# Kernel tuning notes

Measured on AMD Instinct MI355X. Metric: run time of the kernel, lower is better.

## Reference

```python
import jax, jax.numpy as jnp
import numpy as np

N = 4096          # nodes
D_IN = 1024       # in_features
H = 16            # heads
DH = D_IN // H    # d_head
ALPHA = 0.2       # LeakyReLU negative slope
MASK_VAL = -65500.0


def setup_inputs() -> dict:
    key = jax.random.key(0)
    ks = jax.random.split(key, 7)
    x = jax.random.normal(ks[0], (N, D_IN), dtype=jnp.float32)
    adj = jax.random.randint(ks[1], (N, N), 0, 2).astype(jnp.float32)
    s = 1.0 / np.sqrt(D_IN)
    W_seq = jax.random.normal(ks[2], (D_IN, D_IN), dtype=jnp.float32) * s
    a1 = jax.random.normal(ks[3], (DH,), dtype=jnp.float32) / np.sqrt(DH)
    a2 = jax.random.normal(ks[4], (DH,), dtype=jnp.float32) / np.sqrt(DH)
    W_out = jax.random.normal(ks[5], (D_IN, D_IN), dtype=jnp.float32) * s
    b_out = jax.random.normal(ks[6], (D_IN,), dtype=jnp.float32) * 0.01
    return {"x": x, "adj": adj, "W_seq": W_seq, "a1": a1, "a2": a2,
            "W_out": W_out, "b_out": b_out}


def reference(x, adj, W_seq, a1, a2, W_out, b_out):
    # seq: [N, H, DH]
    seq = (x @ W_seq).reshape(N, H, DH)
    # per-head scalar scores: [H, N]
    score1 = jnp.einsum('nhd,d->hn', seq, a1)
    score2 = jnp.einsum('nhd,d->hn', seq, a2)
    # additive attention scores: [H, N, N]
    scores = score1[:, :, None] + score2[:, None, :]
    scores = jax.nn.leaky_relu(scores, negative_slope=ALPHA)
    scores = scores + (1.0 - adj)[None, :, :] * MASK_VAL
    attn = jax.nn.softmax(scores, axis=-1)          # [H, N, N]
    # dropout p=0 -> identity
    hidden = jnp.einsum('hij,jhd->ihd', attn, seq).reshape(N, D_IN)
    hidden = hidden @ W_out + b_out
    # residual=False, concat=True -> ELU
    return jax.nn.elu(hidden)
```

## Files before the change

kernel.cpp:

```cpp
#include <hip/hip_runtime.h>
#include <hip/hip_bf16.h>
#include <math.h>

#define NN 4096
#define DIN 1024
#define NH 16
#define DH 64

typedef unsigned short u16;
typedef unsigned long long u64;
typedef u16 u16x4 __attribute__((ext_vector_type(4)));
typedef u16 u16x8 __attribute__((ext_vector_type(8)));
typedef unsigned ux2 __attribute__((ext_vector_type(2)));
typedef unsigned ux4 __attribute__((ext_vector_type(4)));
typedef float fx4 __attribute__((ext_vector_type(4)));
typedef __bf16 bf16x8 __attribute__((ext_vector_type(8)));
typedef _Float16 h16x8 __attribute__((ext_vector_type(8)));

__device__ __forceinline__ u16 f2b(float f) {
  unsigned u = __float_as_uint(f);
  u += 0x7fff + ((u >> 16) & 1);
  return (u16)(u >> 16);
}
__device__ __forceinline__ float b2f(u16 h) {
  return __uint_as_float(((unsigned)h) << 16);
}
__device__ __forceinline__ u16 f2h_bits(float f) {
  _Float16 h = (_Float16)f;
  return __builtin_bit_cast(unsigned short, h);
}
__device__ __forceinline__ unsigned pack2h(float f) {
  unsigned hb = (unsigned)f2h_bits(f);
  return hb | (hb << 16);
}
__device__ __forceinline__ unsigned pk_mul(unsigned a, unsigned b) {
  unsigned d;
  asm("v_pk_mul_f16 %0, %1, %2" : "=v"(d) : "v"(a), "v"(b));
  return d;
}
__device__ __forceinline__ unsigned pk_max(unsigned a, unsigned b) {
  unsigned d;
  asm("v_pk_max_f16 %0, %1, %2" : "=v"(d) : "v"(a), "v"(b));
  return d;
}
__device__ __forceinline__ void gload16(const void* g, void* l) {
  __builtin_amdgcn_global_load_lds(
      (const __attribute__((address_space(1))) unsigned*)g,
      (__attribute__((address_space(3))) unsigned*)l, 16, 0, 0);
}
__device__ __forceinline__ void wait_vm6() {
  asm volatile("s_waitcnt vmcnt(6)" ::: "memory");
}

__global__ __launch_bounds__(256) void cast_kernel(const float* __restrict__ in,
                                                   u16* __restrict__ out, int n4) {
  int i = blockIdx.x * 256 + threadIdx.x;
  if (i < n4) {
    fx4 v = reinterpret_cast<const fx4*>(in)[i];
    u16x4 o;
    o[0] = f2b(v[0]); o[1] = f2b(v[1]); o[2] = f2b(v[2]); o[3] = f2b(v[3]);
    reinterpret_cast<u16x4*>(out)[i] = o;
  }
}

__global__ __launch_bounds__(256) void tcast_kernel(const float* __restrict__ in,
                                                    u16* __restrict__ out, int R, int C) {
  __shared__ u16 tile[32][33];
  int bc = blockIdx.x * 32, br = blockIdx.y * 32;
  int tx = threadIdx.x & 31, ty = threadIdx.x >> 5;
  #pragma unroll
  for (int r = ty; r < 32; r += 8)
    tile[r][tx] = f2b(in[(size_t)(br + r) * C + bc + tx]);
  __syncthreads();
  #pragma unroll
  for (int r = ty; r < 32; r += 8)
    out[(size_t)(bc + r) * R + br + tx] = tile[tx][r];
}

__global__ __launch_bounds__(256, 2) void gemm_seq(const u16* __restrict__ A,
                                                   const u16* __restrict__ BT,
                                                   const float* __restrict__ a1,
                                                   const float* __restrict__ a2,
                                                   u16* __restrict__ seqTh,
                                                   float* __restrict__ s1T,
                                                   float* __restrict__ s2H,
                                                   int K) {
  __shared__ __align__(16) u16 As[2][128 * 64];
  __shared__ __align__(16) u16 Bs[2][64 * 64];
  const int tid = threadIdx.x;
  const int i0 = blockIdx.x * 128, n0 = blockIdx.y * 64, h = blockIdx.y;
  const int w = tid >> 6, l = tid & 63;
  const int wr = w >> 1, wc = w & 1;
  const int lr = l & 15, lslot = l >> 4;
  const int wu = __builtin_amdgcn_readfirstlane(w);
  const int srow_lo = l >> 3, sg = (l & 7) ^ (srow_lo & 7);
  const u16* gA[4];
  #pragma unroll
  for (int jj = 0; jj < 4; jj++)
    gA[jj] = A + (size_t)(i0 + wu * 32 + jj * 8 + srow_lo) * K + sg * 8;
  const u16* gB[2];
  #pragma unroll
  for (int jb = 0; jb < 2; jb++)
    gB[jb] = BT + (size_t)(n0 + wu * 16 + jb * 8 + srow_lo) * K + sg * 8;

  fx4 acc[4][2] = {};

  #pragma unroll
  for (int jj = 0; jj < 4; jj++)
    gload16(gA[jj], (char*)As[0] + wu * 4096 + jj * 1024);
  #pragma unroll
  for (int jb = 0; jb < 2; jb++)
    gload16(gB[jb], (char*)Bs[0] + wu * 2048 + jb * 1024);
  __syncthreads();

  for (int kt = 0; kt < 16; kt++) {
    const int buf = kt & 1;
    __builtin_amdgcn_s_barrier();
    {
      const int kn = ((kt + 1) & 15) * 64;
      __builtin_amdgcn_sched_barrier(0);
      #pragma unroll
      for (int jj = 0; jj < 4; jj++)
        gload16(gA[jj] + kn, (char*)As[buf ^ 1] + wu * 4096 + jj * 1024);
      #pragma unroll
      for (int jb = 0; jb < 2; jb++)
        gload16(gB[jb] + kn, (char*)Bs[buf ^ 1] + wu * 2048 + jb * 1024);
      __builtin_amdgcn_sched_barrier(0);
      wait_vm6();
      __builtin_amdgcn_sched_barrier(0);
    }
    __builtin_amdgcn_s_barrier();
    #pragma unroll
    for (int ks = 0; ks < 2; ks++) {
      bf16x8 af[4], bfr[2];
      #pragma unroll
      for (int mi = 0; mi < 4; mi++) {
        const int r = wr * 64 + mi * 16 + lr;
        const int sl = (ks * 4 + lslot) ^ (r & 7);
        af[mi] = *reinterpret_cast<const bf16x8*>((const char*)As[buf] + r * 128 + sl * 16);
      }
      #pragma unroll
      for (int ni = 0; ni < 2; ni++) {
        const int r = wc * 32 + ni * 16 + lr;
        const int sl = (ks * 4 + lslot) ^ (r & 7);
        bfr[ni] = *reinterpret_cast<const bf16x8*>((const char*)Bs[buf] + r * 128 + sl * 16);
      }
      #pragma unroll
      for (int mi = 0; mi < 4; mi++)
        #pragma unroll
        for (int ni = 0; ni < 2; ni++)
          acc[mi][ni] = __builtin_amdgcn_mfma_f32_16x16x32_bf16(af[mi], bfr[ni], acc[mi][ni], 0, 0, 0);
    }
  }
  __syncthreads();

  float a1v[2], a2v[2];
  #pragma unroll
  for (int ni = 0; ni < 2; ni++) {
    int dl = wc * 32 + ni * 16 + lr;
    a1v[ni] = a1[dl];
    a2v[ni] = a2[dl];
  }
  #pragma unroll
  for (int mi = 0; mi < 4; mi++)
    #pragma unroll
    for (int r = 0; r < 4; r++) {
      float s1 = acc[mi][0][r] * a1v[0] + acc[mi][1][r] * a1v[1];
      float s2 = acc[mi][0][r] * a2v[0] + acc[mi][1][r] * a2v[1];
      #pragma unroll
      for (int off = 1; off < 16; off <<= 1) {
        s1 += __shfl_xor(s1, off);
        s2 += __shfl_xor(s2, off);
      }
      if (lr == 0) {
        int row = i0 + wr * 64 + mi * 16 + lslot * 4 + r;
        atomicAdd(&s1T[row * NH + h], s1);
        atomicAdd(&s2H[(size_t)h * NN + row], s2);
      }
    }

  u16* tp = (u16*)As;
  #pragma unroll
  for (int mi = 0; mi < 4; mi++)
    #pragma unroll
    for (int ni = 0; ni < 2; ni++)
      #pragma unroll
      for (int rp = 0; rp < 2; rp++) {
        unsigned pw = (unsigned)f2h_bits(acc[mi][ni][2 * rp]) |
                      ((unsigned)f2h_bits(acc[mi][ni][2 * rp + 1]) << 16);
        int d = wc * 32 + ni * 16 + lr;
        int i = wr * 64 + mi * 16 + lslot * 4 + 2 * rp;
        *reinterpret_cast<unsigned*>(&tp[d * 132 + i]) = pw;
      }
  __syncthreads();
  const int dd = tid >> 2, ic = (tid & 3) * 32;
  u16* go = seqTh + (size_t)(h * DH + dd) * NN + i0 + ic;
  #pragma unroll
  for (int q = 0; q < 8; q++) {
    u16x4 v = *reinterpret_cast<const u16x4*>(&tp[dd * 132 + ic + q * 4]);
    *reinterpret_cast<u16x4*>(go + q * 4) = v;
  }
}

__global__ __launch_bounds__(256, 2) void gemm_bt(const u16* __restrict__ A,
                                                  const u16* __restrict__ BT,
                                                  float* __restrict__ Cf,
                                                  const float* __restrict__ bias,
                                                  int M, int N, int K) {
  __shared__ __align__(16) u16 As[2][128 * 64];
  __shared__ __align__(16) u16 Bs[2][64 * 64];
  const int tid = threadIdx.x;
  const int i0 = blockIdx.x * 128, n0 = blockIdx.y * 64;
  const int w = tid >> 6, l = tid & 63;
  const int wr = w >> 1, wc = w & 1;
  const int lr = l & 15, lslot = l >> 4;
  const int wu = __builtin_amdgcn_readfirstlane(w);
  const int srow_lo = l >> 3, sg = (l & 7) ^ (srow_lo & 7);
  const u16* gA[4];
  #pragma unroll
  for (int jj = 0; jj < 4; jj++)
    gA[jj] = A + (size_t)(i0 + wu * 32 + jj * 8 + srow_lo) * K + sg * 8;
  const u16* gB[2];
  #pragma unroll
  for (int jb = 0; jb < 2; jb++)
    gB[jb] = BT + (size_t)(n0 + wu * 16 + jb * 8 + srow_lo) * K + sg * 8;

  fx4 acc[4][2] = {};

  #pragma unroll
  for (int jj = 0; jj < 4; jj++)
    gload16(gA[jj], (char*)As[0] + wu * 4096 + jj * 1024);
  #pragma unroll
  for (int jb = 0; jb < 2; jb++)
    gload16(gB[jb], (char*)Bs[0] + wu * 2048 + jb * 1024);
  __syncthreads();

  for (int kt = 0; kt < 16; kt++) {
    const int buf = kt & 1;
    __builtin_amdgcn_s_barrier();
    {
      const int kn = ((kt + 1) & 15) * 64;
      __builtin_amdgcn_sched_barrier(0);
      #pragma unroll
      for (int jj = 0; jj < 4; jj++)
        gload16(gA[jj] + kn, (char*)As[buf ^ 1] + wu * 4096 + jj * 1024);
      #pragma unroll
      for (int jb = 0; jb < 2; jb++)
        gload16(gB[jb] + kn, (char*)Bs[buf ^ 1] + wu * 2048 + jb * 1024);
      __builtin_amdgcn_sched_barrier(0);
      wait_vm6();
      __builtin_amdgcn_sched_barrier(0);
    }
    __builtin_amdgcn_s_barrier();
    #pragma unroll
    for (int ks = 0; ks < 2; ks++) {
      bf16x8 af[4], bfr[2];
      #pragma unroll
      for (int mi = 0; mi < 4; mi++) {
        const int r = wr * 64 + mi * 16 + lr;
        const int sl = (ks * 4 + lslot) ^ (r & 7);
        af[mi] = *reinterpret_cast<const bf16x8*>((const char*)As[buf] + r * 128 + sl * 16);
      }
      #pragma unroll
      for (int ni = 0; ni < 2; ni++) {
        const int r = wc * 32 + ni * 16 + lr;
        const int sl = (ks * 4 + lslot) ^ (r & 7);
        bfr[ni] = *reinterpret_cast<const bf16x8*>((const char*)Bs[buf] + r * 128 + sl * 16);
      }
      #pragma unroll
      for (int mi = 0; mi < 4; mi++)
        #pragma unroll
        for (int ni = 0; ni < 2; ni++)
          acc[mi][ni] = __builtin_amdgcn_mfma_f32_16x16x32_bf16(af[mi], bfr[ni], acc[mi][ni], 0, 0, 0);
    }
  }

  const int orow = wr * 64 + lslot * 4;
  const int ocol = wc * 32 + lr;
  #pragma unroll
  for (int mi = 0; mi < 4; mi++)
    #pragma unroll
    for (int r = 0; r < 4; r++)
      #pragma unroll
      for (int ni = 0; ni < 2; ni++) {
        int col = n0 + ocol + ni * 16;
        float v = acc[mi][ni][r] + bias[col];
        Cf[(size_t)(i0 + orow + mi * 16 + r) * N + col] = v > 0.f ? v : expm1f(v);
      }
}

__global__ __launch_bounds__(256) void prep_kernel(const float* __restrict__ s2H,
                                                   float* __restrict__ Dmax,
                                                   unsigned* __restrict__ epH2,
                                                   unsigned* __restrict__ enH2) {
  __shared__ float red[4];
  __shared__ float sDm;
  const int h = blockIdx.x, t = threadIdx.x;
  const fx4* d = reinterpret_cast<const fx4*>(s2H + (size_t)h * NN);
  fx4 v[4];
  float mx = -3e38f;
  #pragma unroll
  for (int q = 0; q < 4; q++) {
    v[q] = d[t * 4 + q];
    #pragma unroll
    for (int z = 0; z < 4; z++) mx = fmaxf(mx, v[q][z]);
  }
  #pragma unroll
  for (int off = 1; off < 64; off <<= 1) mx = fmaxf(mx, __shfl_xor(mx, off));
  if ((t & 63) == 0) red[t >> 6] = mx;
  __syncthreads();
  if (t == 0) {
    float m = fmaxf(fmaxf(red[0], red[1]), fmaxf(red[2], red[3]));
    sDm = m;
    Dmax[h] = m;
  }
  __syncthreads();
  const float Dm = sDm;
  #pragma unroll
  for (int q = 0; q < 8; q++) {
    float d0 = v[q >> 1][(q & 1) * 2];
    float d1 = v[q >> 1][(q & 1) * 2 + 1];
    unsigned ep = (unsigned)f2h_bits(__expf(d0 - Dm)) |
                  ((unsigned)f2h_bits(__expf(d1 - Dm)) << 16);
    unsigned en = (unsigned)f2h_bits(__expf(0.2f * (d0 - Dm))) |
                  ((unsigned)f2h_bits(__expf(0.2f * (d1 - Dm))) << 16);
    epH2[h * 2048 + t * 8 + q] = ep;
    enH2[h * 2048 + t * 8 + q] = en;
  }
}

__global__ __launch_bounds__(256) void maskb_kernel(const float* __restrict__ adj,
                                                    unsigned char* __restrict__ mb) {
  size_t g = (size_t)blockIdx.x * 256 + threadIdx.x;
  const fx4* ap = reinterpret_cast<const fx4*>(adj) + g * 4;
  ux4 o;
  #pragma unroll
  for (int q = 0; q < 4; q++) {
    fx4 a = ap[q];
    unsigned b0 = a[0] > 0.5f ? 0xFFu : 0u;
    unsigned b1 = a[1] > 0.5f ? 0xFFu : 0u;
    unsigned b2 = a[2] > 0.5f ? 0xFFu : 0u;
    unsigned b3 = a[3] > 0.5f ? 0xFFu : 0u;
    o[q] = b0 | (b1 << 8) | (b2 << 16) | (b3 << 24);
  }
  reinterpret_cast<ux4*>(mb)[g] = o;
}

__device__ __forceinline__ h16x8 build_p(unsigned Ai2, unsigned Bi2,
                                         ux4 ep, ux4 en, ux2 mk) {
  unsigned w0 = __builtin_amdgcn_perm(0u, mk[0], 0x01010000u);
  unsigned w1 = __builtin_amdgcn_perm(0u, mk[0], 0x03030202u);
  unsigned w2 = __builtin_amdgcn_perm(0u, mk[1], 0x01010000u);
  unsigned w3 = __builtin_amdgcn_perm(0u, mk[1], 0x03030202u);
  ux4 afw;
  afw[0] = pk_max(pk_mul(Ai2, ep[0]), pk_mul(Bi2, en[0])) & w0;
  afw[1] = pk_max(pk_mul(Ai2, ep[1]), pk_mul(Bi2, en[1])) & w1;
  afw[2] = pk_max(pk_mul(Ai2, ep[2]), pk_mul(Bi2, en[2])) & w2;
  afw[3] = pk_max(pk_mul(Ai2, ep[3]), pk_mul(Bi2, en[3])) & w3;
  return __builtin_bit_cast(h16x8, afw);
}

__global__ __launch_bounds__(512, 4) void pv_kernel(const unsigned char* __restrict__ maskB,
                                                    const u16* __restrict__ seqTh,
                                                    const float* __restrict__ s1T,
                                                    const float* __restrict__ Dmax,
                                                    const unsigned* __restrict__ epH2,
                                                    const unsigned* __restrict__ enH2,
                                                    u16* __restrict__ hiddenb) {
  __shared__ __align__(16) u16 Vs[2][64 * 128];
  __shared__ __align__(16) unsigned epL[2048];
  __shared__ __align__(16) unsigned enL[2048];
  const int h = blockIdx.x >> 5, it = blockIdx.x & 31, i0 = it * 128;
  const int t = threadIdx.x, w = t >> 6, l = t & 63;
  const int lr = l & 15, hi = l >> 4, lk = hi * 8;
  const float Dm = Dmax[h];
  const int arow = i0 + w * 16 + lr;
  const float c = s1T[arow * NH + h];
  float mi = c + Dm;
  mi = mi > 0.f ? mi : 0.2f * mi;
  const unsigned Ai2 = pack2h(__expf(c + Dm - mi));
  const unsigned Bi2 = pack2h(__expf(0.2f * (c + Dm) - mi));
  {
    const ux4* gep = reinterpret_cast<const ux4*>(epH2 + h * 2048);
    const ux4* gen = reinterpret_cast<const ux4*>(enH2 + h * 2048);
    ux4 e0 = gep[t];
    ux4 n0 = gen[t];
    *reinterpret_cast<ux4*>(&epL[t * 4]) = e0;
    *reinterpret_cast<ux4*>(&enL[t * 4]) = n0;
  }
  const int wu = __builtin_amdgcn_readfirstlane(w);
  const u16* gsrc[2];
  #pragma unroll
  for (int i = 0; i < 2; i++) {
    int row = wu * 8 + i * 4 + (l >> 4);
    int g = (l & 15) ^ (row & 7);
    gsrc[i] = seqTh + (size_t)(h * DH + row) * NN + g * 8;
  }
  const unsigned char* gm0 = maskB + (size_t)arow * NN + lk;
  fx4 acc[4] = {};
  fx4 acc1 = {};
  h16x8 ones;
  #pragma unroll
  for (int e = 0; e < 8; e++) ones[e] = (_Float16)1.0f;

  #pragma unroll
  for (int i = 0; i < 2; i++)
    gload16(gsrc[i], (char*)Vs[0] + wu * 2048 + i * 1024);
  ux2 mkc[2][2], mkn[2][2];
  #pragma unroll
  for (int jj = 0; jj < 2; jj++)
    #pragma unroll
    for (int ks = 0; ks < 2; ks++)
      mkc[jj][ks] = *reinterpret_cast<const ux2*>(gm0 + jj * 64 + ks * 32);
  __syncthreads();

  for (int JT = 0; JT < 32; JT++) {
    const int buf = JT & 1;
    __builtin_amdgcn_s_barrier();
    {
      const int jn = ((JT + 1) & 31) * 128;
      __builtin_amdgcn_sched_barrier(0);
      #pragma unroll
      for (int i = 0; i < 2; i++)
        gload16(gsrc[i] + jn, (char*)Vs[buf ^ 1] + wu * 2048 + i * 1024);
      #pragma unroll
      for (int jj = 0; jj < 2; jj++)
        #pragma unroll
        for (int ks = 0; ks < 2; ks++)
          mkn[jj][ks] = *reinterpret_cast<const ux2*>(gm0 + jn + jj * 64 + ks * 32);
      __builtin_amdgcn_sched_barrier(0);
      wait_vm6();
      __builtin_amdgcn_sched_barrier(0);
    }
    __builtin_amdgcn_s_barrier();
    #pragma unroll
    for (int jj = 0; jj < 2; jj++) {
      #pragma unroll
      for (int ks = 0; ks < 2; ks++) {
        const int jp = JT * 64 + jj * 32 + ks * 16 + hi * 4;
        ux4 ep = *reinterpret_cast<const ux4*>(&epL[jp]);
        ux4 en = *reinterpret_cast<const ux4*>(&enL[jp]);
        h16x8 bfr[4];
        #pragma unroll
        for (int ni = 0; ni < 4; ni++) {
          const int row = ni * 16 + lr;
          const int colb = (jj * 128 + ks * 64 + hi * 16) ^ ((lr & 7) << 4);
          bfr[ni] = *reinterpret_cast<const h16x8*>((const char*)Vs[buf] + row * 256 + colb);
        }
        h16x8 A = build_p(Ai2, Bi2, ep, en, mkc[jj][ks]);
        #pragma unroll
        for (int ni = 0; ni < 4; ni++)
          acc[ni] = __builtin_amdgcn_mfma_f32_16x16x32_f16(A, bfr[ni], acc[ni], 0, 0, 0);
        acc1 = __builtin_amdgcn_mfma_f32_16x16x32_f16(A, ones, acc1, 0, 0, 0);
      }
    }
    #pragma unroll
    for (int jj = 0; jj < 2; jj++)
      #pragma unroll
      for (int ks = 0; ks < 2; ks++)
        mkc[jj][ks] = mkn[jj][ks];
  }

  #pragma unroll
  for (int r = 0; r < 4; r++) {
    int row = i0 + w * 16 + hi * 4 + r;
    float inv = 1.0f / acc1[r];
    #pragma unroll
    for (int ni = 0; ni < 4; ni++)
      hiddenb[(size_t)row * DIN + h * DH + ni * 16 + lr] = f2b(acc[ni][r] * inv);
  }
}

extern "C" void kernel_launch(void* const* d_in, const int* in_sizes, int n_in,
                              void* d_out, int out_size, void* d_ws, size_t ws_size,
                              hipStream_t stream) {
  const float* x = (const float*)d_in[0];
  const float* adj = (const float*)d_in[1];
  const float* W_seq = (const float*)d_in[2];
  const float* a1 = (const float*)d_in[3];
  const float* a2 = (const float*)d_in[4];
  const float* W_out = (const float*)d_in[5];
  const float* b_out = (const float*)d_in[6];

  char* ws = (char*)d_ws;
  u16* wsT   = (u16*)(ws);
  u16* woT   = (u16*)(ws + (2u << 20));
  u16* seqTh = (u16*)(ws + (12u << 20));
  u16* hid   = (u16*)(ws + (20u << 20));
  float* s1T = (float*)(ws + (28u << 20));
  float* s2H = s1T + NN * NH;
  unsigned* epH2 = (unsigned*)(s2H + NN * NH);
  unsigned* enH2 = epH2 + NH * 2048;
  float* DmaxB = (float*)(enH2 + NH * 2048);
  u16* xb = (u16*)(ws + (29u << 20));
  unsigned char* maskB = (unsigned char*)(ws + (29u << 20));

  cast_kernel<<<4096, 256, 0, stream>>>(x, xb, NN * DIN / 4);
  tcast_kernel<<<dim3(32, 32), 256, 0, stream>>>(W_seq, wsT, DIN, DIN);
  tcast_kernel<<<dim3(32, 32), 256, 0, stream>>>(W_out, woT, DIN, DIN);
  hipMemsetAsync(s1T, 0, 2u * NN * NH * sizeof(float), stream);
  gemm_seq<<<dim3(32, 16), 256, 0, stream>>>(xb, wsT, a1, a2, seqTh, s1T, s2H, DIN);
  prep_kernel<<<16, 256, 0, stream>>>(s2H, DmaxB, epH2, enH2);
  maskb_kernel<<<4096, 256, 0, stream>>>(adj, maskB);
  pv_kernel<<<512, 512, 0, stream>>>(maskB, seqTh, s1T, DmaxB, epH2, enH2, hid);
  gemm_bt<<<dim3(32, 16), 256, 0, stream>>>(hid, woT, (float*)d_out, b_out, NN, DIN, DIN);
}
```

Baseline: 148.6 us.

## Process two row tiles per wave in PV kernel to reuse V fragments

Each wave in the attention-times-V kernel now handles 32 query rows (two 16-row M tiles) instead of 16. This halves the grid to 256 blocks and reuses each V fragment read from LDS across two MFMA chains. The main loop is unrolled by two with explicit ping-pong buffers, which removes the mask register copy, and the waitcnt is raised to match the larger number of outstanding loads. The cost is higher register pressure (launch bounds drop to 2 blocks per CU) and only 256 blocks, which may underfill the MI355X's 256 CUs.

```diff
diff --git a/kernel.cpp b/kernel.cpp
--- a/kernel.cpp
+++ b/kernel.cpp
@@ -50,6 +50,9 @@
 }
 __device__ __forceinline__ void wait_vm6() {
   asm volatile("s_waitcnt vmcnt(6)" ::: "memory");
+}
+__device__ __forceinline__ void wait_vm10() {
+  asm volatile("s_waitcnt vmcnt(10)" ::: "memory");
 }
 
 __global__ __launch_bounds__(256) void cast_kernel(const float* __restrict__ in,
@@ -360,7 +363,7 @@
   return __builtin_bit_cast(h16x8, afw);
 }
 
-__global__ __launch_bounds__(512, 4) void pv_kernel(const unsigned char* __restrict__ maskB,
+__global__ __launch_bounds__(512, 2) void pv_kernel(const unsigned char* __restrict__ maskB,
                                                     const u16* __restrict__ seqTh,
                                                     const float* __restrict__ s1T,
                                                     const float* __restrict__ Dmax,
@@ -370,16 +373,22 @@
   __shared__ __align__(16) u16 Vs[2][64 * 128];
   __shared__ __align__(16) unsigned epL[2048];
   __shared__ __align__(16) unsigned enL[2048];
-  const int h = blockIdx.x >> 5, it = blockIdx.x & 31, i0 = it * 128;
+  const int h = blockIdx.x >> 4, it = blockIdx.x & 15, i0 = it * 256;
   const int t = threadIdx.x, w = t >> 6, l = t & 63;
   const int lr = l & 15, hi = l >> 4, lk = hi * 8;
   const float Dm = Dmax[h];
-  const int arow = i0 + w * 16 + lr;
-  const float c = s1T[arow * NH + h];
-  float mi = c + Dm;
-  mi = mi > 0.f ? mi : 0.2f * mi;
-  const unsigned Ai2 = pack2h(__expf(c + Dm - mi));
-  const unsigned Bi2 = pack2h(__expf(0.2f * (c + Dm) - mi));
+  unsigned Ai2[2], Bi2[2];
+  int arow[2];
+  #pragma unroll
+  for (int m = 0; m < 2; m++) {
+    int row = i0 + w * 32 + m * 16 + lr;
+    arow[m] = row;
+    float c = s1T[row * NH + h];
+    float mi = c + Dm;
+    mi = mi > 0.f ? mi : 0.2f * mi;
+    Ai2[m] = pack2h(__expf(c + Dm - mi));
+    Bi2[m] = pack2h(__expf(0.2f * (c + Dm) - mi));
+  }
   {
     const ux4* gep = reinterpret_cast<const ux4*>(epH2 + h * 2048);
     const ux4* gen = reinterpret_cast<const ux4*>(enH2 + h * 2048);
@@ -396,43 +405,34 @@
     int g = (l & 15) ^ (row & 7);
     gsrc[i] = seqTh + (size_t)(h * DH + row) * NN + g * 8;
   }
-  const unsigned char* gm0 = maskB + (size_t)arow * NN + lk;
-  fx4 acc[4] = {};
-  fx4 acc1 = {};
+  const unsigned char* gm[2];
+  gm[0] = maskB + (size_t)arow[0] * NN + lk;
+  gm[1] = maskB + (size_t)arow[1] * NN + lk;
+  fx4 acc[2][4] = {};
+  fx4 acc1[2] = {};
   h16x8 ones;
   #pragma unroll
   for (int e = 0; e < 8; e++) ones[e] = (_Float16)1.0f;
 
-  #pragma unroll
-  for (int i = 0; i < 2; i++)
-    gload16(gsrc[i], (char*)Vs[0] + wu * 2048 + i * 1024);
-  ux2 mkc[2][2], mkn[2][2];
-  #pragma unroll
-  for (int jj = 0; jj < 2; jj++)
-    #pragma unroll
-    for (int ks = 0; ks < 2; ks++)
-      mkc[jj][ks] = *reinterpret_cast<const ux2*>(gm0 + jj * 64 + ks * 32);
-  __syncthreads();
-
-  for (int JT = 0; JT < 32; JT++) {
-    const int buf = JT & 1;
-    __builtin_amdgcn_s_barrier();
-    {
-      const int jn = ((JT + 1) & 31) * 128;
-      __builtin_amdgcn_sched_barrier(0);
-      #pragma unroll
-      for (int i = 0; i < 2; i++)
-        gload16(gsrc[i] + jn, (char*)Vs[buf ^ 1] + wu * 2048 + i * 1024);
+  ux2 mkA[2][2][2], mkB[2][2][2];
+
+  auto issue = [&](int JTn, u16* vbuf, ux2 (&mk)[2][2][2]) {
+    const int jn = JTn * 128;
+    __builtin_amdgcn_sched_barrier(0);
+    #pragma unroll
+    for (int i = 0; i < 2; i++)
+      gload16(gsrc[i] + jn, (char*)vbuf + wu * 2048 + i * 1024);
+    #pragma unroll
+    for (int m = 0; m < 2; m++)
       #pragma unroll
       for (int jj = 0; jj < 2; jj++)
         #pragma unroll
         for (int ks = 0; ks < 2; ks++)
-          mkn[jj][ks] = *reinterpret_cast<const ux2*>(gm0 + jn + jj * 64 + ks * 32);
-      __builtin_amdgcn_sched_barrier(0);
-      wait_vm6();
-      __builtin_amdgcn_sched_barrier(0);
-    }
-    __builtin_amdgcn_s_barrier();
+          mk[m][jj][ks] = *reinterpret_cast<const ux2*>(gm[m] + jn + jj * 64 + ks * 32);
+    __builtin_amdgcn_sched_barrier(0);
+  };
+
+  auto compute = [&](int JT, const u16* vbuf, const ux2 (&mk)[2][2][2]) {
     #pragma unroll
     for (int jj = 0; jj < 2; jj++) {
       #pragma unroll
@@ -445,30 +445,49 @@
         for (int ni = 0; ni < 4; ni++) {
           const int row = ni * 16 + lr;
           const int colb = (jj * 128 + ks * 64 + hi * 16) ^ ((lr & 7) << 4);
-          bfr[ni] = *reinterpret_cast<const h16x8*>((const char*)Vs[buf] + row * 256 + colb);
+          bfr[ni] = *reinterpret_cast<const h16x8*>((const char*)vbuf + row * 256 + colb);
         }
-        h16x8 A = build_p(Ai2, Bi2, ep, en, mkc[jj][ks]);
         #pragma unroll
-        for (int ni = 0; ni < 4; ni++)
-          acc[ni] = __builtin_amdgcn_mfma_f32_16x16x32_f16(A, bfr[ni], acc[ni], 0, 0, 0);
-        acc1 = __builtin_amdgcn_mfma_f32_16x16x32_f16(A, ones, acc1, 0, 0, 0);
-      }
-    }
-    #pragma unroll
-    for (int jj = 0; jj < 2; jj++)
-      #pragma unroll
-      for (int ks = 0; ks < 2; ks++)
-        mkc[jj][ks] = mkn[jj][ks];
-  }
-
-  #pragma unroll
-  for (int r = 0; r < 4; r++) {
-    int row = i0 + w * 16 + hi * 4 + r;
-    float inv = 1.0f / acc1[r];
-    #pragma unroll
-    for (int ni = 0; ni < 4; ni++)
-      hiddenb[(size_t)row * DIN + h * DH + ni * 16 + lr] = f2b(acc[ni][r] * inv);
-  }
+        for (int m = 0; m < 2; m++) {
+          h16x8 A = build_p(Ai2[m], Bi2[m], ep, en, mk[m][jj][ks]);
+          #pragma unroll
+          for (int ni = 0; ni < 4; ni++)
+            acc[m][ni] = __builtin_amdgcn_mfma_f32_16x16x32_f16(A, bfr[ni], acc[m][ni], 0, 0, 0);
+          acc1[m] = __builtin_amdgcn_mfma_f32_16x16x32_f16(A, ones, acc1[m], 0, 0, 0);
+        }
+      }
+    }
+  };
+
+  issue(0, Vs[0], mkA);
+  __syncthreads();
+
+  for (int JT2 = 0; JT2 < 16; JT2++) {
+    const int JTa = JT2 * 2, JTb = JTa + 1;
+    __builtin_amdgcn_s_barrier();
+    issue(JTb, Vs[1], mkB);
+    wait_vm10();
+    __builtin_amdgcn_sched_barrier(0);
+    __builtin_amdgcn_s_barrier();
+    compute(JTa, Vs[0], mkA);
+    __builtin_amdgcn_s_barrier();
+    issue((JTb + 1) & 31, Vs[0], mkA);
+    wait_vm10();
+    __builtin_amdgcn_sched_barrier(0);
+    __builtin_amdgcn_s_barrier();
+    compute(JTb, Vs[1], mkB);
+  }
+
+  #pragma unroll
+  for (int m = 0; m < 2; m++)
+    #pragma unroll
+    for (int r = 0; r < 4; r++) {
+      int row = i0 + w * 32 + m * 16 + hi * 4 + r;
+      float inv = 1.0f / acc1[m][r];
+      #pragma unroll
+      for (int ni = 0; ni < 4; ni++)
+        hiddenb[(size_t)row * DIN + h * DH + ni * 16 + lr] = f2b(acc[m][ni][r] * inv);
+    }
 }
 
 extern "C" void kernel_launch(void* const* d_in, const int* in_sizes, int n_in,
@@ -502,6 +521,6 @@
   gemm_seq<<<dim3(32, 16), 256, 0, stream>>>(xb, wsT, a1, a2, seqTh, s1T, s2H, DIN);
   prep_kernel<<<16, 256, 0, stream>>>(s2H, DmaxB, epH2, enH2);
   maskb_kernel<<<4096, 256, 0, stream>>>(adj, maskB);
-  pv_kernel<<<512, 512, 0, stream>>>(maskB, seqTh, s1T, DmaxB, epH2, enH2, hid);
+  pv_kernel<<<256, 512, 0, stream>>>(maskB, seqTh, s1T, DmaxB, epH2, enH2, hid);
   gemm_bt<<<dim3(32, 16), 256, 0, stream>>>(hid, woT, (float*)d_out, b_out, NN, DIN, DIN);
 }
```

New measurement: 171.0 us. 15.1% more time.

## Split PV key tile across wave pairs, each wave covering two row groups

Applied to the files above, without the earlier changes.

The PV kernel's wave-to-work mapping changes. Each wave now handles two 16-row groups over half of the 128-key tile, where before it handled one 16-row group over the full tile. Each V fragment loaded from LDS is reused across two row groups, roughly halving LDS reads of V per MFMA. The cost is doubled accumulator registers and a final LDS reduction step with extra barriers to combine the two key halves before normalization.

```diff
diff --git a/kernel.cpp b/kernel.cpp
--- a/kernel.cpp
+++ b/kernel.cpp
@@ -372,14 +372,21 @@
   __shared__ __align__(16) unsigned enL[2048];
   const int h = blockIdx.x >> 5, it = blockIdx.x & 31, i0 = it * 128;
   const int t = threadIdx.x, w = t >> 6, l = t & 63;
+  const int rg = w >> 1, jh = w & 1;
   const int lr = l & 15, hi = l >> 4, lk = hi * 8;
   const float Dm = Dmax[h];
-  const int arow = i0 + w * 16 + lr;
-  const float c = s1T[arow * NH + h];
-  float mi = c + Dm;
-  mi = mi > 0.f ? mi : 0.2f * mi;
-  const unsigned Ai2 = pack2h(__expf(c + Dm - mi));
-  const unsigned Bi2 = pack2h(__expf(0.2f * (c + Dm) - mi));
+  unsigned Ai2[2], Bi2[2];
+  int arow[2];
+  #pragma unroll
+  for (int m = 0; m < 2; m++) {
+    int row = i0 + rg * 32 + m * 16 + lr;
+    arow[m] = row;
+    float c = s1T[row * NH + h];
+    float mi = c + Dm;
+    mi = mi > 0.f ? mi : 0.2f * mi;
+    Ai2[m] = pack2h(__expf(c + Dm - mi));
+    Bi2[m] = pack2h(__expf(0.2f * (c + Dm) - mi));
+  }
   {
     const ux4* gep = reinterpret_cast<const ux4*>(epH2 + h * 2048);
     const ux4* gen = reinterpret_cast<const ux4*>(enH2 + h * 2048);
@@ -396,9 +403,11 @@
     int g = (l & 15) ^ (row & 7);
     gsrc[i] = seqTh + (size_t)(h * DH + row) * NN + g * 8;
   }
-  const unsigned char* gm0 = maskB + (size_t)arow * NN + lk;
-  fx4 acc[4] = {};
-  fx4 acc1 = {};
+  const unsigned char* gm[2];
+  gm[0] = maskB + (size_t)arow[0] * NN + jh * 64 + lk;
+  gm[1] = maskB + (size_t)arow[1] * NN + jh * 64 + lk;
+  fx4 acc[2][4] = {};
+  fx4 acc1[2] = {};
   h16x8 ones;
   #pragma unroll
   for (int e = 0; e < 8; e++) ones[e] = (_Float16)1.0f;
@@ -408,10 +417,10 @@
     gload16(gsrc[i], (char*)Vs[0] + wu * 2048 + i * 1024);
   ux2 mkc[2][2], mkn[2][2];
   #pragma unroll
-  for (int jj = 0; jj < 2; jj++)
+  for (int m = 0; m < 2; m++)
     #pragma unroll
     for (int ks = 0; ks < 2; ks++)
-      mkc[jj][ks] = *reinterpret_cast<const ux2*>(gm0 + jj * 64 + ks * 32);
+      mkc[m][ks] = *reinterpret_cast<const ux2*>(gm[m] + ks * 32);
   __syncthreads();
 
   for (int JT = 0; JT < 32; JT++) {
@@ -424,50 +433,73 @@
       for (int i = 0; i < 2; i++)
         gload16(gsrc[i] + jn, (char*)Vs[buf ^ 1] + wu * 2048 + i * 1024);
       #pragma unroll
-      for (int jj = 0; jj < 2; jj++)
+      for (int m = 0; m < 2; m++)
         #pragma unroll
         for (int ks = 0; ks < 2; ks++)
-          mkn[jj][ks] = *reinterpret_cast<const ux2*>(gm0 + jn + jj * 64 + ks * 32);
+          mkn[m][ks] = *reinterpret_cast<const ux2*>(gm[m] + jn + ks * 32);
       __builtin_amdgcn_sched_barrier(0);
       wait_vm6();
       __builtin_amdgcn_sched_barrier(0);
     }
     __builtin_amdgcn_s_barrier();
     #pragma unroll
-    for (int jj = 0; jj < 2; jj++) {
-      #pragma unroll
-      for (int ks = 0; ks < 2; ks++) {
-        const int jp = JT * 64 + jj * 32 + ks * 16 + hi * 4;
-        ux4 ep = *reinterpret_cast<const ux4*>(&epL[jp]);
-        ux4 en = *reinterpret_cast<const ux4*>(&enL[jp]);
-        h16x8 bfr[4];
-        #pragma unroll
-        for (int ni = 0; ni < 4; ni++) {
-          const int row = ni * 16 + lr;
-          const int colb = (jj * 128 + ks * 64 + hi * 16) ^ ((lr & 7) << 4);
-          bfr[ni] = *reinterpret_cast<const h16x8*>((const char*)Vs[buf] + row * 256 + colb);
-        }
-        h16x8 A = build_p(Ai2, Bi2, ep, en, mkc[jj][ks]);
+    for (int ks = 0; ks < 2; ks++) {
+      const int jp = JT * 64 + jh * 32 + ks * 16 + hi * 4;
+      ux4 ep = *reinterpret_cast<const ux4*>(&epL[jp]);
+      ux4 en = *reinterpret_cast<const ux4*>(&enL[jp]);
+      h16x8 bfr[4];
+      #pragma unroll
+      for (int ni = 0; ni < 4; ni++) {
+        const int row = ni * 16 + lr;
+        const int colb = (jh * 128 + ks * 64 + hi * 16) ^ ((lr & 7) << 4);
+        bfr[ni] = *reinterpret_cast<const h16x8*>((const char*)Vs[buf] + row * 256 + colb);
+      }
+      #pragma unroll
+      for (int m = 0; m < 2; m++) {
+        h16x8 A = build_p(Ai2[m], Bi2[m], ep, en, mkc[m][ks]);
         #pragma unroll
         for (int ni = 0; ni < 4; ni++)
-          acc[ni] = __builtin_amdgcn_mfma_f32_16x16x32_f16(A, bfr[ni], acc[ni], 0, 0, 0);
-        acc1 = __builtin_amdgcn_mfma_f32_16x16x32_f16(A, ones, acc1, 0, 0, 0);
-      }
-    }
-    #pragma unroll
-    for (int jj = 0; jj < 2; jj++)
+          acc[m][ni] = __builtin_amdgcn_mfma_f32_16x16x32_f16(A, bfr[ni], acc[m][ni], 0, 0, 0);
+        acc1[m] = __builtin_amdgcn_mfma_f32_16x16x32_f16(A, ones, acc1[m], 0, 0, 0);
+      }
+    }
+    #pragma unroll
+    for (int m = 0; m < 2; m++)
       #pragma unroll
       for (int ks = 0; ks < 2; ks++)
-        mkc[jj][ks] = mkn[jj][ks];
-  }
-
-  #pragma unroll
-  for (int r = 0; r < 4; r++) {
-    int row = i0 + w * 16 + hi * 4 + r;
-    float inv = 1.0f / acc1[r];
-    #pragma unroll
-    for (int ni = 0; ni < 4; ni++)
-      hiddenb[(size_t)row * DIN + h * DH + ni * 16 + lr] = f2b(acc[ni][r] * inv);
+        mkc[m][ks] = mkn[m][ks];
+  }
+
+  __syncthreads();
+  fx4* sA = reinterpret_cast<fx4*>(Vs);
+  fx4* sB = reinterpret_cast<fx4*>(epL);
+  const int base = rg * 64 + l;
+  if (jh == 1) {
+    #pragma unroll
+    for (int m = 0; m < 2; m++) {
+      #pragma unroll
+      for (int ni = 0; ni < 4; ni++)
+        sA[base * 8 + m * 4 + ni] = acc[m][ni];
+      sB[base * 2 + m] = acc1[m];
+    }
+  }
+  __syncthreads();
+  if (jh == 0) {
+    #pragma unroll
+    for (int m = 0; m < 2; m++) {
+      #pragma unroll
+      for (int ni = 0; ni < 4; ni++)
+        acc[m][ni] += sA[base * 8 + m * 4 + ni];
+      acc1[m] += sB[base * 2 + m];
+      #pragma unroll
+      for (int r = 0; r < 4; r++) {
+        int row = i0 + rg * 32 + m * 16 + hi * 4 + r;
+        float inv = 1.0f / acc1[m][r];
+        #pragma unroll
+        for (int ni = 0; ni < 4; ni++)
+          hiddenb[(size_t)row * DIN + h * DH + ni * 16 + lr] = f2b(acc[m][ni][r] * inv);
+      }
+    }
   }
 }
 
```

Result: no change. 150.9 us (+1.5%).

## Triple-buffer V tiles in pv_kernel with two-step prefetch distance

Applied to the files above, without the earlier changes.

The attention-value kernel moves from double to triple buffering of the V tile in LDS. Global-to-LDS loads are now issued two iterations ahead, the adjacency mask one iteration ahead, and the wait threshold is relaxed from vmcnt(6) to vmcnt(8) to hide more memory latency. This grows per-block LDS by a third, which may cut resident blocks per CU. Selecting the mask registers with a runtime JT&1 index could also add selects or scratch traffic.

```diff
diff --git a/kernel.cpp b/kernel.cpp
--- a/kernel.cpp
+++ b/kernel.cpp
@@ -50,6 +50,9 @@
 }
 __device__ __forceinline__ void wait_vm6() {
   asm volatile("s_waitcnt vmcnt(6)" ::: "memory");
+}
+__device__ __forceinline__ void wait_vm8() {
+  asm volatile("s_waitcnt vmcnt(8)" ::: "memory");
 }
 
 __global__ __launch_bounds__(256) void cast_kernel(const float* __restrict__ in,
@@ -367,7 +370,7 @@
                                                     const unsigned* __restrict__ epH2,
                                                     const unsigned* __restrict__ enH2,
                                                     u16* __restrict__ hiddenb) {
-  __shared__ __align__(16) u16 Vs[2][64 * 128];
+  __shared__ __align__(16) u16 Vs[3][64 * 128];
   __shared__ __align__(16) unsigned epL[2048];
   __shared__ __align__(16) unsigned enL[2048];
   const int h = blockIdx.x >> 5, it = blockIdx.x & 31, i0 = it * 128;
@@ -403,36 +406,43 @@
   #pragma unroll
   for (int e = 0; e < 8; e++) ones[e] = (_Float16)1.0f;
 
+  ux2 mkS[2][2][2];
+
+  #pragma unroll
+  for (int jj = 0; jj < 2; jj++)
+    #pragma unroll
+    for (int ks = 0; ks < 2; ks++)
+      mkS[0][jj][ks] = *reinterpret_cast<const ux2*>(gm0 + jj * 64 + ks * 32);
   #pragma unroll
   for (int i = 0; i < 2; i++)
     gload16(gsrc[i], (char*)Vs[0] + wu * 2048 + i * 1024);
-  ux2 mkc[2][2], mkn[2][2];
-  #pragma unroll
-  for (int jj = 0; jj < 2; jj++)
-    #pragma unroll
-    for (int ks = 0; ks < 2; ks++)
-      mkc[jj][ks] = *reinterpret_cast<const ux2*>(gm0 + jj * 64 + ks * 32);
+  #pragma unroll
+  for (int i = 0; i < 2; i++)
+    gload16(gsrc[i] + 128, (char*)Vs[1] + wu * 2048 + i * 1024);
   __syncthreads();
 
   for (int JT = 0; JT < 32; JT++) {
-    const int buf = JT & 1;
     __builtin_amdgcn_s_barrier();
     {
-      const int jn = ((JT + 1) & 31) * 128;
-      __builtin_amdgcn_sched_barrier(0);
-      #pragma unroll
-      for (int i = 0; i < 2; i++)
-        gload16(gsrc[i] + jn, (char*)Vs[buf ^ 1] + wu * 2048 + i * 1024);
+      const int jm = ((JT + 1) & 31) * 128;
+      const int jg = ((JT + 2) & 31) * 128;
+      u16* vdst = (u16*)Vs[(JT + 2) % 3];
+      __builtin_amdgcn_sched_barrier(0);
       #pragma unroll
       for (int jj = 0; jj < 2; jj++)
         #pragma unroll
         for (int ks = 0; ks < 2; ks++)
-          mkn[jj][ks] = *reinterpret_cast<const ux2*>(gm0 + jn + jj * 64 + ks * 32);
-      __builtin_amdgcn_sched_barrier(0);
-      wait_vm6();
+          mkS[(JT + 1) & 1][jj][ks] =
+              *reinterpret_cast<const ux2*>(gm0 + jm + jj * 64 + ks * 32);
+      #pragma unroll
+      for (int i = 0; i < 2; i++)
+        gload16(gsrc[i] + jg, (char*)vdst + wu * 2048 + i * 1024);
+      __builtin_amdgcn_sched_barrier(0);
+      wait_vm8();
       __builtin_amdgcn_sched_barrier(0);
     }
     __builtin_amdgcn_s_barrier();
+    const u16* vbuf = Vs[JT % 3];
     #pragma unroll
     for (int jj = 0; jj < 2; jj++) {
       #pragma unroll
@@ -445,20 +455,15 @@
         for (int ni = 0; ni < 4; ni++) {
           const int row = ni * 16 + lr;
           const int colb = (jj * 128 + ks * 64 + hi * 16) ^ ((lr & 7) << 4);
-          bfr[ni] = *reinterpret_cast<const h16x8*>((const char*)Vs[buf] + row * 256 + colb);
+          bfr[ni] = *reinterpret_cast<const h16x8*>((const char*)vbuf + row * 256 + colb);
         }
-        h16x8 A = build_p(Ai2, Bi2, ep, en, mkc[jj][ks]);
+        h16x8 A = build_p(Ai2, Bi2, ep, en, mkS[JT & 1][jj][ks]);
         #pragma unroll
         for (int ni = 0; ni < 4; ni++)
           acc[ni] = __builtin_amdgcn_mfma_f32_16x16x32_f16(A, bfr[ni], acc[ni], 0, 0, 0);
         acc1 = __builtin_amdgcn_mfma_f32_16x16x32_f16(A, ones, acc1, 0, 0, 0);
       }
     }
-    #pragma unroll
-    for (int jj = 0; jj < 2; jj++)
-      #pragma unroll
-      for (int ks = 0; ks < 2; ks++)
-        mkc[jj][ks] = mkn[jj][ks];
   }
 
   #pragma unroll
```

Result: slower. 165.2 us (+11.2%).
